# Performance work log

Hardware: AMD Instinct MI355X
Metric: run time of the kernel (lower is better)

The kernel has to match this reference:

```python
import jax, jax.numpy as jnp
import numpy as np

TEMP = 11.313708498984761  # sqrt(head_dim=128)

def setup_inputs() -> dict:
    key = jax.random.key(0)
    kq, kk, kv, km = jax.random.split(key, 4)
    B, H, S, D = 2, 16, 2048, 128
    q = jax.random.normal(kq, (B, H, S, D), dtype=jnp.float32)
    k = jax.random.normal(kk, (B, H, S, D), dtype=jnp.float32)
    v = jax.random.normal(kv, (B, H, S, D), dtype=jnp.float32)
    mask = jax.random.randint(km, (B, 1, S, S), 0, 2, dtype=jnp.int32)
    return {"q": q, "k": k, "v": v, "mask": mask}

def reference(q, k, v, mask):
    # atten = (q / temp) @ k^T  -> [B,H,S,S]
    atten = jnp.einsum("bhsd,bhtd->bhst", q / TEMP, k)
    maskf = mask.astype(atten.dtype)
    # torch masked_fill_(mask.bool(), 1e-9): positions where mask != 0 get 1e-9
    atten = jnp.where(mask.astype(bool), jnp.asarray(1e-9, atten.dtype), atten)
    atten = jax.nn.softmax(atten, axis=-1)
    # then multiply by mask (zeros out mask==0 positions)
    atten = atten * maskf
    # dropout: eval mode (identity) for a deterministic correctness baseline
    out = jnp.einsum("bhst,bhtd->bhsd", atten, v)
    return (out, atten)
```

## Files before the change

### kernel.cpp

```cpp
#include <hip/hip_runtime.h>
#include <stdint.h>

#define B_ 2
#define H_ 16
#define S_ 2048
#define D_ 128

typedef float f32x4 __attribute__((ext_vector_type(4)));
typedef short bf16x8 __attribute__((ext_vector_type(8)));
typedef unsigned short u16x4 __attribute__((ext_vector_type(4)));
typedef int i32x4 __attribute__((ext_vector_type(4)));

__device__ __forceinline__ unsigned short f2bf(float x){
  union { float f; uint32_t u; } c; c.f = x;
  uint32_t u = c.u;
  uint32_t r = (u + 0x7FFFu + ((u >> 16) & 1u)) >> 16;
  return (unsigned short)r;
}

__global__ void kconv_kernel(const float* __restrict__ k, unsigned short* __restrict__ KB){
  size_t i = (size_t)blockIdx.x * 256 + threadIdx.x;
  f32x4 v = __builtin_nontemporal_load(&((const f32x4*)k)[i]);
  u16x4 o; o[0]=f2bf(v.x); o[1]=f2bf(v.y); o[2]=f2bf(v.z); o[3]=f2bf(v.w);
  __builtin_nontemporal_store(o, &((u16x4*)KB)[i]);
}

__global__ void vtrans_kernel(const float* __restrict__ v, unsigned short* __restrict__ VT){
  __shared__ float tile[64][73];
  int blk = blockIdx.x;
  int bh = blk >> 6;
  int ts = (blk >> 1) & 31;
  int dsec = blk & 1;
  int t0 = ts*64, d0 = dsec*64;
  const float* vb = v + ((size_t)bh*S_ + t0)*D_ + d0;
  int tid = threadIdx.x;
  #pragma unroll
  for (int i=0;i<4;++i){
    int fi = i*256 + tid;
    int r = fi >> 4;
    int c4 = (fi & 15) * 4;
    f32x4 val = __builtin_nontemporal_load((const f32x4*)(vb + (size_t)r*D_ + c4));
    tile[r][c4+0]=val.x; tile[r][c4+1]=val.y; tile[r][c4+2]=val.z; tile[r][c4+3]=val.w;
  }
  __syncthreads();
  unsigned short* ob = VT + ((size_t)bh*D_ + d0)*S_ + t0;
  #pragma unroll
  for (int i=0;i<4;++i){
    int ui = i*256 + tid;
    int dr = ui >> 4;
    int tc = (ui & 15) * 4;
    u16x4 o;
    o[0] = f2bf(tile[tc+0][dr]);
    o[1] = f2bf(tile[tc+1][dr]);
    o[2] = f2bf(tile[tc+2][dr]);
    o[3] = f2bf(tile[tc+3][dr]);
    __builtin_nontemporal_store(o, (u16x4*)(ob + (size_t)dr*S_ + tc));
  }
}

__global__ void maskprep_kernel(const int* __restrict__ mask, unsigned long long* __restrict__ bits){
  int row = blockIdx.x;
  const int* mrow = mask + (size_t)row*S_;
  int w = threadIdx.x >> 6;
  int lane = threadIdx.x & 63;
  #pragma unroll
  for (int i=0;i<8;++i){
    int t = i*256 + threadIdx.x;
    unsigned long long bm = __ballot(__builtin_nontemporal_load(&mrow[t]) != 0);
    if (lane == 0) bits[(size_t)row*32 + i*4 + w] = bm;
  }
}

__launch_bounds__(512, 4)
__global__ void fused_kernel(const float* __restrict__ q,
                             const unsigned long long* __restrict__ bits,
                             const unsigned short* __restrict__ KB,
                             const unsigned short* __restrict__ VT,
                             float* __restrict__ outp,
                             float* __restrict__ c_ws)
{
  __shared__ unsigned char Ksm[64*256];
  __shared__ unsigned char Vsm[128*128];
  const int tid = threadIdx.x;
  const int lane = tid & 63;
  const int w = tid >> 6;
  const int l16 = lane & 15;
  const int lhi = lane >> 4;

  const int orig = blockIdx.x;
  const int blk = (orig & 7) * 64 + (orig >> 3);
  const int bh = blk >> 4;
  const int qt = blk & 15;
  const int b = bh >> 4;
  const int s0 = qt * 128;
  const int rowbase = s0 + 16*w;

  const float QS = 1.4426950408889634f / 11.313708498984761f;

  bf16x8 qf[4];
  {
    const float* qp = q + ((size_t)bh*S_ + (rowbase + l16))*D_ + lhi*8;
    #pragma unroll
    for (int ks=0; ks<4; ++ks){
      f32x4 a0 = __builtin_nontemporal_load((const f32x4*)(qp + 32*ks));
      f32x4 a1 = __builtin_nontemporal_load((const f32x4*)(qp + 32*ks + 4));
      bf16x8 f;
      f[0]=(short)f2bf(a0.x*QS); f[1]=(short)f2bf(a0.y*QS);
      f[2]=(short)f2bf(a0.z*QS); f[3]=(short)f2bf(a0.w*QS);
      f[4]=(short)f2bf(a1.x*QS); f[5]=(short)f2bf(a1.y*QS);
      f[6]=(short)f2bf(a1.z*QS); f[7]=(short)f2bf(a1.w*QS);
      qf[ks] = f;
    }
  }

  f32x4 Wacc[8];
  #pragma unroll
  for (int dc=0;dc<8;++dc){ f32x4 z = {0.f,0.f,0.f,0.f}; Wacc[dc] = z; }
  float lrow[4] = {0.f,0.f,0.f,0.f};

  const unsigned short* Kg = KB + (size_t)bh*S_*D_;
  const unsigned short* Vg = VT + (size_t)bh*D_*S_;
  const unsigned long long* bitsb = bits + (size_t)b*S_*32;

  int kr[2], kcb[2], vr[2], vcb[2];
  #pragma unroll
  for (int i=0;i<2;++i){
    int chunk = i*512 + tid;
    kr[i] = chunk >> 4;  kcb[i] = (chunk & 15) << 4;
    vr[i] = chunk >> 3;  vcb[i] = (chunk & 7) << 4;
  }
  i32x4 kst[2], vst[2];

  auto loadstage = [&](int it){
    const unsigned char* ksrc = (const unsigned char*)Kg + (size_t)it*64*256;
    const unsigned char* vsrc = (const unsigned char*)(Vg + (size_t)it*64);
    #pragma unroll
    for (int i=0;i<2;++i)
      kst[i] = *(const i32x4*)(ksrc + (size_t)kr[i]*256 + kcb[i]);
    #pragma unroll
    for (int i=0;i<2;++i)
      vst[i] = *(const i32x4*)(vsrc + (size_t)vr[i]*(S_*2) + vcb[i]);
  };
  auto writestage = [&](){
    #pragma unroll
    for (int i=0;i<2;++i)
      *(i32x4*)(&Ksm[kr[i]*256 + (kcb[i] ^ ((kr[i]&7)<<4))]) = kst[i];
    #pragma unroll
    for (int i=0;i<2;++i)
      *(i32x4*)(&Vsm[vr[i]*128 + (vcb[i] ^ ((vr[i]&7)<<4))]) = vst[i];
  };

  loadstage(0);

  for (int it=0; it<32; ++it){
    const int t0 = it*64;
    __syncthreads();
    writestage();

    unsigned long long mbA = bitsb[(size_t)(rowbase + l16)*32 + it];
    unsigned long long mbC[4];
    #pragma unroll
    for (int reg=0; reg<4; ++reg)
      mbC[reg] = bitsb[(size_t)(rowbase + 4*lhi + reg)*32 + it];

    if (it+1 < 32) loadstage(it+1);

    asm volatile("s_waitcnt lgkmcnt(0)" ::: "memory");
    __builtin_amdgcn_sched_barrier(0);
    __builtin_amdgcn_s_barrier();
    __builtin_amdgcn_sched_barrier(0);

    f32x4 Sacc[4];
    #pragma unroll
    for (int cf=0;cf<4;++cf){ f32x4 z = {0.f,0.f,0.f,0.f}; Sacc[cf] = z; }
    __builtin_amdgcn_s_setprio(1);
    #pragma unroll
    for (int cf=0; cf<4; ++cf){
      int t_l = 16*cf + l16;
      #pragma unroll
      for (int ks=0; ks<4; ++ks){
        int cb = 64*ks + lhi*16;
        bf16x8 bfr = *(const bf16x8*)(&Ksm[t_l*256 + (cb ^ ((t_l&7)<<4))]);
        Sacc[cf] = __builtin_amdgcn_mfma_f32_16x16x32_bf16(qf[ks], bfr, Sacc[cf], 0,0,0);
      }
    }
    __builtin_amdgcn_s_setprio(0);

    #pragma unroll
    for (int reg=0; reg<4; ++reg){
      uint32_t lo = (uint32_t)mbC[reg];
      uint32_t hi = (uint32_t)(mbC[reg] >> 32);
      uint32_t a = lo >> l16;
      uint32_t d = hi >> l16;
      float x0 = (a & 1u)        ? 0.f : Sacc[0][reg];
      float x1 = ((a >> 16) & 1u)? 0.f : Sacc[1][reg];
      float x2 = (d & 1u)        ? 0.f : Sacc[2][reg];
      float x3 = ((d >> 16) & 1u)? 0.f : Sacc[3][reg];
      float e0 = __builtin_amdgcn_exp2f(x0);
      float e1 = __builtin_amdgcn_exp2f(x1);
      float e2 = __builtin_amdgcn_exp2f(x2);
      float e3 = __builtin_amdgcn_exp2f(x3);
      lrow[reg] += (e0+e1)+(e2+e3);
    }

    #pragma unroll
    for (int ksw=0; ksw<2; ++ksw){
      uint32_t word = (uint32_t)(mbA >> (32*ksw));
      uint32_t bt = (word >> (8*lhi)) & 0xFFu;
      union { bf16x8 v; uint32_t u[4]; } pk;
      pk.u[0] = (((bt>>0)&1u) | (((bt>>1)&1u)<<16)) * 0x3F80u;
      pk.u[1] = (((bt>>2)&1u) | (((bt>>3)&1u)<<16)) * 0x3F80u;
      pk.u[2] = (((bt>>4)&1u) | (((bt>>5)&1u)<<16)) * 0x3F80u;
      pk.u[3] = (((bt>>6)&1u) | (((bt>>7)&1u)<<16)) * 0x3F80u;
      __builtin_amdgcn_s_setprio(1);
      #pragma unroll
      for (int dc=0; dc<8; ++dc){
        int d_l = 16*dc + l16;
        int cb = 64*ksw + lhi*16;
        bf16x8 bfr = *(const bf16x8*)(&Vsm[d_l*128 + (cb ^ ((d_l&7)<<4))]);
        Wacc[dc] = __builtin_amdgcn_mfma_f32_16x16x32_bf16(pk.v, bfr, Wacc[dc], 0,0,0);
      }
      __builtin_amdgcn_s_setprio(0);
    }
  }

  float cval[4];
  #pragma unroll
  for (int reg=0;reg<4;++reg){
    float l = lrow[reg];
    l += __shfl_xor(l, 1);
    l += __shfl_xor(l, 2);
    l += __shfl_xor(l, 4);
    l += __shfl_xor(l, 8);
    float c = 1.0f / l;
    cval[reg] = c;
    if (l16 == 0){
      c_ws[(size_t)bh*S_ + rowbase + 4*lhi + reg] = c;
    }
  }
  #pragma unroll
  for (int dc=0;dc<8;++dc){
    #pragma unroll
    for (int reg=0;reg<4;++reg){
      int srow = rowbase + 4*lhi + reg;
      __builtin_nontemporal_store(cval[reg]*Wacc[dc][reg],
                                  &outp[((size_t)bh*S_ + srow)*D_ + 16*dc + l16]);
    }
  }
}

__global__ void atten_kernel(const unsigned long long* __restrict__ bits,
                             const float* __restrict__ c_ws,
                             float* __restrict__ atten){
  int blk = blockIdx.x;
  int bq = blk >> 11;
  int s  = blk & 2047;
  __shared__ float csm[16];
  if (threadIdx.x < 16)
    csm[threadIdx.x] = c_ws[((size_t)(bq*H_ + threadIdx.x))*S_ + s];
  __syncthreads();
  const unsigned long long* wrow = bits + ((size_t)bq*S_ + s)*32;
  for (int i = threadIdx.x; i < S_/4; i += 256){
    unsigned long long wv = wrow[i >> 4];
    uint32_t nib = (uint32_t)(wv >> ((i & 15)*4)) & 0xFu;
    #pragma unroll
    for (int h=0; h<H_; ++h){
      float c = csm[h];
      f32x4 o = { (nib&1u)?c:0.f, (nib&2u)?c:0.f, (nib&4u)?c:0.f, (nib&8u)?c:0.f };
      __builtin_nontemporal_store(o, ((f32x4*)(atten + (((size_t)(bq*H_ + h)*S_ + s)*S_))) + i);
    }
  }
}

extern "C" void kernel_launch(void* const* d_in, const int* in_sizes, int n_in,
                              void* d_out, int out_size, void* d_ws, size_t ws_size,
                              hipStream_t stream){
  const float* q = (const float*)d_in[0];
  const float* k = (const float*)d_in[1];
  const float* v = (const float*)d_in[2];
  const int* mask = (const int*)d_in[3];
  float* outp = (float*)d_out;
  float* atten = outp + (size_t)B_*H_*S_*D_;

  unsigned short* KB = (unsigned short*)d_ws;
  unsigned short* VT = KB + (size_t)B_*H_*S_*D_;
  float* c_ws = (float*)(VT + (size_t)B_*H_*S_*D_);
  unsigned long long* bits = (unsigned long long*)(c_ws + (size_t)B_*H_*S_);

  hipLaunchKernelGGL(maskprep_kernel, dim3(4096), dim3(256), 0, stream, mask, bits);
  hipLaunchKernelGGL(kconv_kernel,  dim3(8192), dim3(256), 0, stream, k, KB);
  hipLaunchKernelGGL(vtrans_kernel, dim3(2048), dim3(256), 0, stream, v, VT);
  hipLaunchKernelGGL(fused_kernel,  dim3(512),  dim3(512), 0, stream, q, bits, KB, VT, outp, c_ws);
  hipLaunchKernelGGL(atten_kernel,  dim3(4096), dim3(256), 0, stream, bits, c_ws, atten);
}
```

Before: 265.5 us.

## Switch fused attention kernel to 32x32x16 MFMA with 2x2 wave tiling

Replaces the 16x16x32 MFMA tiling, where each wave owned 16 query rows across all 64 keys and all 128 head dims, with 32x32x16 MFMAs. Waves are now arranged as four row groups by two column halves: each wave computes a 32x32 score block and a 32x64 output slice. The K and V shared-memory layouts and XOR swizzles are reworked to match, and partial row sums are combined across wave pairs through shared memory. The goal is fewer MFMA and LDS instructions per tile, plus fewer mask-bit loads per iteration. In exchange it adds a cross-wave reduction and a block-wide sync at the end, and raises register pressure from the 16-wide accumulators.

```diff
diff --git a/kernel.cpp b/kernel.cpp
--- a/kernel.cpp
+++ b/kernel.cpp
@@ -7,6 +7,7 @@
 #define D_ 128
 
 typedef float f32x4 __attribute__((ext_vector_type(4)));
+typedef float f32x16 __attribute__((ext_vector_type(16)));
 typedef short bf16x8 __attribute__((ext_vector_type(8)));
 typedef unsigned short u16x4 __attribute__((ext_vector_type(4)));
 typedef int i32x4 __attribute__((ext_vector_type(4)));
@@ -79,13 +80,14 @@
                              float* __restrict__ outp,
                              float* __restrict__ c_ws)
 {
-  __shared__ unsigned char Ksm[64*256];
-  __shared__ unsigned char Vsm[128*128];
+  __shared__ __align__(16) unsigned char Ksm[64*256];
+  __shared__ __align__(16) unsigned char Vsm[64*256];
+  __shared__ float lred[8][32];
   const int tid = threadIdx.x;
   const int lane = tid & 63;
   const int w = tid >> 6;
-  const int l16 = lane & 15;
-  const int lhi = lane >> 4;
+  const int l32 = lane & 31;
+  const int lh = lane >> 5;
 
   const int orig = blockIdx.x;
   const int blk = (orig & 7) * 64 + (orig >> 3);
@@ -93,76 +95,77 @@
   const int qt = blk & 15;
   const int b = bh >> 4;
   const int s0 = qt * 128;
-  const int rowbase = s0 + 16*w;
+  const int r = w >> 1;
+  const int cQ = w & 1;
+  const int qrow = s0 + 32*r + l32;
 
   const float QS = 1.4426950408889634f / 11.313708498984761f;
 
-  bf16x8 qf[4];
+  bf16x8 qf[8];
   {
-    const float* qp = q + ((size_t)bh*S_ + (rowbase + l16))*D_ + lhi*8;
-    #pragma unroll
-    for (int ks=0; ks<4; ++ks){
-      f32x4 a0 = __builtin_nontemporal_load((const f32x4*)(qp + 32*ks));
-      f32x4 a1 = __builtin_nontemporal_load((const f32x4*)(qp + 32*ks + 4));
+    const float* qp = q + ((size_t)bh*S_ + qrow)*D_ + 8*lh;
+    #pragma unroll
+    for (int m=0; m<8; ++m){
+      f32x4 a0 = __builtin_nontemporal_load((const f32x4*)(qp + 16*m));
+      f32x4 a1 = __builtin_nontemporal_load((const f32x4*)(qp + 16*m + 4));
       bf16x8 f;
       f[0]=(short)f2bf(a0.x*QS); f[1]=(short)f2bf(a0.y*QS);
       f[2]=(short)f2bf(a0.z*QS); f[3]=(short)f2bf(a0.w*QS);
       f[4]=(short)f2bf(a1.x*QS); f[5]=(short)f2bf(a1.y*QS);
       f[6]=(short)f2bf(a1.z*QS); f[7]=(short)f2bf(a1.w*QS);
-      qf[ks] = f;
-    }
-  }
-
-  f32x4 Wacc[8];
-  #pragma unroll
-  for (int dc=0;dc<8;++dc){ f32x4 z = {0.f,0.f,0.f,0.f}; Wacc[dc] = z; }
-  float lrow[4] = {0.f,0.f,0.f,0.f};
-
-  const unsigned short* Kg = KB + (size_t)bh*S_*D_;
-  const unsigned short* Vg = VT + (size_t)bh*D_*S_;
-  const unsigned long long* bitsb = bits + (size_t)b*S_*32;
-
-  int kr[2], kcb[2], vr[2], vcb[2];
+      qf[m] = f;
+    }
+  }
+
+  f32x16 Wacc[2];
+  #pragma unroll
+  for (int n=0;n<2;++n)
+    #pragma unroll
+    for (int e=0;e<16;++e) Wacc[n][e] = 0.f;
+  float lsum = 0.f;
+
+  const unsigned char* Kgb = (const unsigned char*)(KB + (size_t)bh*S_*D_);
+  const unsigned char* Vgb = (const unsigned char*)(VT + (size_t)bh*D_*S_);
+  const unsigned long long* bitsb = bits + (size_t)b*S_*32 + (size_t)qrow*32;
+
+  int kr_[2], kcb_[2], vrow_[2], vslot_[2]; size_t vsrc_[2];
   #pragma unroll
   for (int i=0;i<2;++i){
-    int chunk = i*512 + tid;
-    kr[i] = chunk >> 4;  kcb[i] = (chunk & 15) << 4;
-    vr[i] = chunk >> 3;  vcb[i] = (chunk & 7) << 4;
+    int c = i*512 + tid;
+    kr_[i]  = c >> 4;
+    kcb_[i] = c & 15;
+    int d   = c >> 3;
+    int ts  = c & 7;
+    vrow_[i]  = d >> 1;
+    vslot_[i] = ((d&1)<<3) | ts;
+    vsrc_[i]  = (size_t)d*(S_*2) + ts*16;
   }
   i32x4 kst[2], vst[2];
 
   auto loadstage = [&](int it){
-    const unsigned char* ksrc = (const unsigned char*)Kg + (size_t)it*64*256;
-    const unsigned char* vsrc = (const unsigned char*)(Vg + (size_t)it*64);
     #pragma unroll
     for (int i=0;i<2;++i)
-      kst[i] = *(const i32x4*)(ksrc + (size_t)kr[i]*256 + kcb[i]);
+      kst[i] = *(const i32x4*)(Kgb + (size_t)it*16384 + kr_[i]*256 + (kcb_[i]<<4));
     #pragma unroll
     for (int i=0;i<2;++i)
-      vst[i] = *(const i32x4*)(vsrc + (size_t)vr[i]*(S_*2) + vcb[i]);
+      vst[i] = *(const i32x4*)(Vgb + vsrc_[i] + (size_t)it*128);
   };
   auto writestage = [&](){
     #pragma unroll
     for (int i=0;i<2;++i)
-      *(i32x4*)(&Ksm[kr[i]*256 + (kcb[i] ^ ((kr[i]&7)<<4))]) = kst[i];
+      *(i32x4*)(&Ksm[kr_[i]*256 + ((kcb_[i] ^ (kr_[i]&15))<<4)]) = kst[i];
     #pragma unroll
     for (int i=0;i<2;++i)
-      *(i32x4*)(&Vsm[vr[i]*128 + (vcb[i] ^ ((vr[i]&7)<<4))]) = vst[i];
+      *(i32x4*)(&Vsm[vrow_[i]*256 + ((vslot_[i] ^ (vrow_[i]&15))<<4)]) = vst[i];
   };
 
   loadstage(0);
 
   for (int it=0; it<32; ++it){
-    const int t0 = it*64;
     __syncthreads();
     writestage();
 
-    unsigned long long mbA = bitsb[(size_t)(rowbase + l16)*32 + it];
-    unsigned long long mbC[4];
-    #pragma unroll
-    for (int reg=0; reg<4; ++reg)
-      mbC[reg] = bitsb[(size_t)(rowbase + 4*lhi + reg)*32 + it];
-
+    unsigned long long mb = bitsb[it];
     if (it+1 < 32) loadstage(it+1);
 
     asm volatile("s_waitcnt lgkmcnt(0)" ::: "memory");
@@ -170,81 +173,84 @@
     __builtin_amdgcn_s_barrier();
     __builtin_amdgcn_sched_barrier(0);
 
-    f32x4 Sacc[4];
-    #pragma unroll
-    for (int cf=0;cf<4;++cf){ f32x4 z = {0.f,0.f,0.f,0.f}; Sacc[cf] = z; }
+    f32x16 Sacc;
+    #pragma unroll
+    for (int e=0;e<16;++e) Sacc[e] = 0.f;
+    const int trow = 32*cQ + l32;
+    const int tbase = trow*256;
+    const int txr = trow & 15;
     __builtin_amdgcn_s_setprio(1);
     #pragma unroll
-    for (int cf=0; cf<4; ++cf){
-      int t_l = 16*cf + l16;
+    for (int m=0; m<8; ++m){
+      int slot = (2*m + lh) ^ txr;
+      bf16x8 kf = *(const bf16x8*)(&Ksm[tbase + (slot<<4)]);
+      Sacc = __builtin_amdgcn_mfma_f32_32x32x16_bf16(kf, qf[m], Sacc, 0,0,0);
+    }
+    __builtin_amdgcn_s_setprio(0);
+
+    uint32_t mw = (uint32_t)(mb >> (32*cQ + 4*lh));
+    #pragma unroll
+    for (int reg=0; reg<16; ++reg){
+      const int tb = (reg&3) + 8*(reg>>2);
+      float x = ((mw >> tb) & 1u) ? 0.f : Sacc[reg];
+      lsum += __builtin_amdgcn_exp2f(x);
+    }
+
+    unsigned long long ms = mb >> (8*lh);
+    uint32_t mlo = (uint32_t)ms, mhi = (uint32_t)(ms >> 32);
+    bf16x8 am[4];
+    #pragma unroll
+    for (int m2=0; m2<4; ++m2){
+      uint32_t bt = ((m2 < 2 ? mlo : mhi) >> (16*(m2&1))) & 0xFFu;
+      union { bf16x8 v; uint32_t u[4]; } pk;
       #pragma unroll
-      for (int ks=0; ks<4; ++ks){
-        int cb = 64*ks + lhi*16;
-        bf16x8 bfr = *(const bf16x8*)(&Ksm[t_l*256 + (cb ^ ((t_l&7)<<4))]);
-        Sacc[cf] = __builtin_amdgcn_mfma_f32_16x16x32_bf16(qf[ks], bfr, Sacc[cf], 0,0,0);
+      for (int j2=0; j2<4; ++j2){
+        pk.u[j2] = (((bt>>(2*j2))&1u) ? 0x3F80u : 0u)
+                 | (((bt>>(2*j2+1))&1u) ? 0x3F800000u : 0u);
       }
-    }
-    __builtin_amdgcn_s_setprio(0);
-
-    #pragma unroll
-    for (int reg=0; reg<4; ++reg){
-      uint32_t lo = (uint32_t)mbC[reg];
-      uint32_t hi = (uint32_t)(mbC[reg] >> 32);
-      uint32_t a = lo >> l16;
-      uint32_t d = hi >> l16;
-      float x0 = (a & 1u)        ? 0.f : Sacc[0][reg];
-      float x1 = ((a >> 16) & 1u)? 0.f : Sacc[1][reg];
-      float x2 = (d & 1u)        ? 0.f : Sacc[2][reg];
-      float x3 = ((d >> 16) & 1u)? 0.f : Sacc[3][reg];
-      float e0 = __builtin_amdgcn_exp2f(x0);
-      float e1 = __builtin_amdgcn_exp2f(x1);
-      float e2 = __builtin_amdgcn_exp2f(x2);
-      float e3 = __builtin_amdgcn_exp2f(x3);
-      lrow[reg] += (e0+e1)+(e2+e3);
-    }
-
-    #pragma unroll
-    for (int ksw=0; ksw<2; ++ksw){
-      uint32_t word = (uint32_t)(mbA >> (32*ksw));
-      uint32_t bt = (word >> (8*lhi)) & 0xFFu;
-      union { bf16x8 v; uint32_t u[4]; } pk;
-      pk.u[0] = (((bt>>0)&1u) | (((bt>>1)&1u)<<16)) * 0x3F80u;
-      pk.u[1] = (((bt>>2)&1u) | (((bt>>3)&1u)<<16)) * 0x3F80u;
-      pk.u[2] = (((bt>>4)&1u) | (((bt>>5)&1u)<<16)) * 0x3F80u;
-      pk.u[3] = (((bt>>6)&1u) | (((bt>>7)&1u)<<16)) * 0x3F80u;
+      am[m2] = pk.v;
+    }
+
+    #pragma unroll
+    for (int n=0; n<2; ++n){
+      const int dd = 32*(2*cQ + n) + l32;
+      const int vbase = (dd>>1)*256;
+      const int vx = (dd&1)<<3;
+      const int vxr = (dd>>1)&15;
       __builtin_amdgcn_s_setprio(1);
       #pragma unroll
-      for (int dc=0; dc<8; ++dc){
-        int d_l = 16*dc + l16;
-        int cb = 64*ksw + lhi*16;
-        bf16x8 bfr = *(const bf16x8*)(&Vsm[d_l*128 + (cb ^ ((d_l&7)<<4))]);
-        Wacc[dc] = __builtin_amdgcn_mfma_f32_16x16x32_bf16(pk.v, bfr, Wacc[dc], 0,0,0);
+      for (int m2=0; m2<4; ++m2){
+        int slot = (vx | (2*m2 + lh)) ^ vxr;
+        bf16x8 vf = *(const bf16x8*)(&Vsm[vbase + (slot<<4)]);
+        Wacc[n] = __builtin_amdgcn_mfma_f32_32x32x16_bf16(am[m2], vf, Wacc[n], 0,0,0);
       }
       __builtin_amdgcn_s_setprio(0);
     }
   }
 
-  float cval[4];
-  #pragma unroll
-  for (int reg=0;reg<4;++reg){
-    float l = lrow[reg];
-    l += __shfl_xor(l, 1);
-    l += __shfl_xor(l, 2);
-    l += __shfl_xor(l, 4);
-    l += __shfl_xor(l, 8);
-    float c = 1.0f / l;
-    cval[reg] = c;
-    if (l16 == 0){
-      c_ws[(size_t)bh*S_ + rowbase + 4*lhi + reg] = c;
-    }
-  }
-  #pragma unroll
-  for (int dc=0;dc<8;++dc){
-    #pragma unroll
-    for (int reg=0;reg<4;++reg){
-      int srow = rowbase + 4*lhi + reg;
-      __builtin_nontemporal_store(cval[reg]*Wacc[dc][reg],
-                                  &outp[((size_t)bh*S_ + srow)*D_ + 16*dc + l16]);
+  lsum += __shfl_xor(lsum, 32);
+  if (lane < 32) lred[w][l32] = lsum;
+  __syncthreads();
+
+  float cval[16];
+  #pragma unroll
+  for (int reg=0; reg<16; ++reg){
+    int crow = (reg&3) + 8*(reg>>2) + 4*lh;
+    cval[reg] = 1.0f / (lred[2*r][crow] + lred[2*r+1][crow]);
+  }
+  if (tid < 128){
+    int rr = tid >> 5;
+    float cc = 1.0f / (lred[2*rr][tid&31] + lred[2*rr+1][tid&31]);
+    c_ws[(size_t)bh*S_ + s0 + tid] = cc;
+  }
+  #pragma unroll
+  for (int n=0; n<2; ++n){
+    const int dd = 32*(2*cQ + n) + l32;
+    #pragma unroll
+    for (int reg=0; reg<16; ++reg){
+      int row = s0 + 32*r + (reg&3) + 8*(reg>>2) + 4*lh;
+      __builtin_nontemporal_store(cval[reg]*Wacc[n][reg],
+                                  &outp[((size_t)bh*S_ + row)*D_ + dd]);
     }
   }
 }
```

After: 348.3 us. +31.2%, slower.
